# Performance work log

Hardware: AMD Instinct MI355X
Metric: run time of the kernel (lower is better)

## Reference

```python
import jax, jax.numpy as jnp
import numpy as np

FRAME = 1024
ENC = 256
HID = 128
EPS = 1e-7


def _lstm_cell(x, h, c, Wih, Whh, bih, bhh):
    # PyTorch LSTM gate order: i, f, g, o
    z = Wih @ x + bih + Whh @ h + bhh  # [4H]
    i, f, g, o = jnp.split(z, 4)
    i = jax.nn.sigmoid(i)
    f = jax.nn.sigmoid(f)
    g = jnp.tanh(g)
    o = jax.nn.sigmoid(o)
    c_new = f * c + i * g
    h_new = o * jnp.tanh(c_new)
    return h_new, c_new


def setup_inputs() -> dict:
    key = jax.random.key(0)
    ks = jax.random.split(key, 20)
    s = 0.05
    return {
        "y1": jax.random.normal(ks[0], (FRAME,), jnp.float32),
        "h1_in": jax.random.normal(ks[1], (HID,), jnp.float32),
        "c1_in": jax.random.normal(ks[2], (HID,), jnp.float32),
        "h2_in": jax.random.normal(ks[3], (HID,), jnp.float32),
        "c2_in": jax.random.normal(ks[4], (HID,), jnp.float32),
        "enc_W": jax.random.normal(ks[5], (ENC, FRAME), jnp.float32) * s,
        "gamma": jnp.ones((ENC,), jnp.float32),
        "beta": jnp.zeros((ENC,), jnp.float32),
        "Wih1": jax.random.normal(ks[6], (4 * HID, ENC), jnp.float32) * s,
        "Whh1": jax.random.normal(ks[7], (4 * HID, HID), jnp.float32) * s,
        "bih1": jax.random.normal(ks[8], (4 * HID,), jnp.float32) * s,
        "bhh1": jax.random.normal(ks[9], (4 * HID,), jnp.float32) * s,
        "Wih2": jax.random.normal(ks[10], (4 * HID, HID), jnp.float32) * s,
        "Whh2": jax.random.normal(ks[11], (4 * HID, HID), jnp.float32) * s,
        "bih2": jax.random.normal(ks[12], (4 * HID,), jnp.float32) * s,
        "bhh2": jax.random.normal(ks[13], (4 * HID,), jnp.float32) * s,
        "dense_W": jax.random.normal(ks[14], (ENC, HID), jnp.float32) * s,
        "dense_b": jax.random.normal(ks[15], (ENC,), jnp.float32) * s,
        "dec_W": jax.random.normal(ks[16], (FRAME, ENC), jnp.float32) * s,
    }


def reference(y1, h1_in, c1_in, h2_in, c2_in, enc_W, gamma, beta,
              Wih1, Whh1, bih1, bhh1, Wih2, Whh2, bih2, bhh2,
              dense_W, dense_b, dec_W):
    # encoder 1x1 conv == matvec: [256,1024] @ [1024]
    enc = enc_W @ y1  # [256]
    # global-statistic instant layer norm (mean/var over ALL elements)
    mean = jnp.mean(enc)
    sub = enc - mean
    var = jnp.mean(jnp.square(sub))
    enc_norm = (sub / jnp.sqrt(var + EPS)) * gamma + beta
    # two stateful LSTM cells (seq_len=1; dropout is identity at inference)
    h1, c1 = _lstm_cell(enc_norm, h1_in, c1_in, Wih1, Whh1, bih1, bhh1)
    h2, c2 = _lstm_cell(h1, h2_in, c2_in, Wih2, Whh2, bih2, bhh2)
    # dense + sigmoid mask on UN-normalized encoded features
    mask = jax.nn.sigmoid(dense_W @ h2 + dense_b)  # [256]
    estimated = mask * enc
    # decoder 1x1 conv == matvec: [1024,256] @ [256]
    decoded = dec_W @ estimated  # [1024]
    return (decoded.reshape(1, FRAME, 1),
            h1.reshape(1, 1, HID), c1.reshape(1, 1, HID),
            h2.reshape(1, 1, HID), c2.reshape(1, 1, HID))
```

## Files before the change

### kernel.cpp

```cpp
#include <hip/hip_runtime.h>
#include <math.h>


#define FRAME 1024
#define ENC 256
#define HID 128
#define MSTRIDE 32

__device__ __forceinline__ float sigmoidf_(float x) { return 1.0f / (1.0f + __expf(-x)); }
__device__ __forceinline__ float tanhf_(float x) { return 2.0f * sigmoidf_(2.0f * x) - 1.0f; }

__device__ __forceinline__ float wred(float v) {
#pragma unroll
    for (int o = 32; o > 0; o >>= 1) v += __shfl_xor(v, o);
    return v;
}

__global__ __launch_bounds__(256) void k_enc(
    const float* __restrict__ enc_W, const float* __restrict__ y1,
    const float* __restrict__ Whh1, const float* __restrict__ bih1,
    const float* __restrict__ bhh1, const float* __restrict__ h1_in,
    const float* __restrict__ Whh2, const float* __restrict__ bih2,
    const float* __restrict__ bhh2, const float* __restrict__ h2_in,
    float* __restrict__ enc_g, float* __restrict__ ph1,
    float* __restrict__ ph2, float* __restrict__ macc) {
    const int t = threadIdx.x, lane = t & 63, w = t >> 6, bid = blockIdx.x;
    if (bid < 256) {
        const float4 a = reinterpret_cast<const float4*>(enc_W + bid * FRAME)[t];
        const float4 b = reinterpret_cast<const float4*>(y1)[t];
        float p = a.x * b.x + a.y * b.y + a.z * b.z + a.w * b.w;
        p = wred(p);
        __shared__ float red[4];
        if (lane == 0) red[w] = p;
        __syncthreads();
        if (t == 0) enc_g[bid] = red[0] + red[1] + red[2] + red[3];
    } else {
        const bool is1 = bid < 288;
        const int pb = is1 ? bid - 256 : bid - 288;
        const float* Whh = is1 ? Whh1 : Whh2;
        const float* bi  = is1 ? bih1 : bih2;
        const float* bh  = is1 ? bhh1 : bhh2;
        const float* hin = is1 ? h1_in : h2_in;
        float* dst       = is1 ? ph1 : ph2;
        const float2 hv = reinterpret_cast<const float2*>(hin)[lane];
#pragma unroll
        for (int j = 0; j < 4; ++j) {
            const int r = pb * 16 + w * 4 + j;
            const float2 a = reinterpret_cast<const float2*>(Whh + r * HID)[lane];
            float p = a.x * hv.x + a.y * hv.y;
            p = wred(p);
            if (lane == 0) dst[r] = p + bi[r] + bh[r];
        }
        if (!is1 && t < 8) macc[(pb * 8 + t) * MSTRIDE] = 0.0f;
    }
}

__global__ __launch_bounds__(256) void k_z1(
    const float* __restrict__ enc_g, const float* __restrict__ gamma,
    const float* __restrict__ beta, const float* __restrict__ Wih1,
    const float* __restrict__ ph1, const float* __restrict__ c1_in,
    float* __restrict__ h1_g, float* __restrict__ out) {
    const int t = threadIdx.x, lane = t & 63, w = t >> 6, b = blockIdx.x;
    __shared__ __align__(16) float encN[ENC];
    __shared__ float red[8];
    __shared__ float zsh[4];

    const int r = b + HID * w;
    const float4 wa = reinterpret_cast<const float4*>(Wih1 + r * ENC)[lane];
    const float ph = ph1[r];

    const float e = enc_g[t];
    const float s1 = wred(e);
    const float s2 = wred(e * e);
    if (lane == 0) { red[w] = s1; red[4 + w] = s2; }
    __syncthreads();
    const float mean = (red[0] + red[1] + red[2] + red[3]) * (1.f / ENC);
    const float var  = (red[4] + red[5] + red[6] + red[7]) * (1.f / ENC) - mean * mean;
    const float inv  = rsqrtf(var + 1e-7f);
    encN[t] = (e - mean) * inv * gamma[t] + beta[t];
    __syncthreads();

    const float4 xa = reinterpret_cast<const float4*>(encN)[lane];
    float p = wa.x * xa.x + wa.y * xa.y + wa.z * xa.z + wa.w * xa.w;
    p = wred(p);
    if (lane == 0) zsh[w] = p + ph;
    __syncthreads();
    if (t == 0) {
        const float i = sigmoidf_(zsh[0]);
        const float f = sigmoidf_(zsh[1]);
        const float g = tanhf_(zsh[2]);
        const float o = sigmoidf_(zsh[3]);
        const float c = f * c1_in[b] + i * g;
        const float h = o * tanhf_(c);
        h1_g[b] = h;
        out[FRAME + b] = h;
        out[FRAME + HID + b] = c;
    }
}

__global__ __launch_bounds__(256) void k_z2(
    const float* __restrict__ h1_g, const float* __restrict__ Wih2,
    const float* __restrict__ ph2, const float* __restrict__ c2_in,
    const float* __restrict__ dense_W, float* __restrict__ macc,
    float* __restrict__ out) {
    const int t = threadIdx.x, lane = t & 63, w = t >> 6, bid = blockIdx.x;
    const int ub = bid * 4;
    __shared__ __align__(16) float hA[HID];
    __shared__ float zsh[16];
    __shared__ float h2sh[4];

    const float4 dcol = *reinterpret_cast<const float4*>(dense_W + t * HID + ub);
    float2 wa[4]; float phv[4];
#pragma unroll
    for (int j = 0; j < 4; ++j) {
        const int r = (ub + j) + HID * w;
        wa[j] = reinterpret_cast<const float2*>(Wih2 + r * HID)[lane];
        phv[j] = ph2[r];
    }

    if (t < HID) hA[t] = h1_g[t];
    __syncthreads();
    const float2 xa = reinterpret_cast<const float2*>(hA)[lane];
#pragma unroll
    for (int j = 0; j < 4; ++j) {
        float p = wa[j].x * xa.x + wa[j].y * xa.y;
        p = wred(p);
        if (lane == 0) zsh[w * 4 + j] = p + phv[j];
    }
    __syncthreads();
    if (t < 4) {
        const int u = ub + t;
        const float i = sigmoidf_(zsh[0 * 4 + t]);
        const float f = sigmoidf_(zsh[1 * 4 + t]);
        const float g = tanhf_(zsh[2 * 4 + t]);
        const float o = sigmoidf_(zsh[3 * 4 + t]);
        const float c = f * c2_in[u] + i * g;
        const float h = o * tanhf_(c);
        h2sh[t] = h;
        out[FRAME + 2 * HID + u] = h;
        out[FRAME + 3 * HID + u] = c;
    }
    __syncthreads();
    const float contrib = dcol.x * h2sh[0] + dcol.y * h2sh[1]
                        + dcol.z * h2sh[2] + dcol.w * h2sh[3];
    atomicAdd(&macc[t * MSTRIDE], contrib);
}

__global__ __launch_bounds__(256) void k_dec(
    const float* __restrict__ dec_W, const float* __restrict__ macc,
    const float* __restrict__ dense_b, const float* __restrict__ enc_g,
    float* __restrict__ out) {
    const int t = threadIdx.x, lane = t & 63, w = t >> 6;
    __shared__ __align__(16) float es[ENC];
    const float m = macc[t * MSTRIDE];
    es[t] = sigmoidf_(m + dense_b[t]) * enc_g[t];
    __syncthreads();
    const int r = blockIdx.x * 4 + w;
    const float4 a = reinterpret_cast<const float4*>(dec_W + r * ENC)[lane];
    const float4 bb = reinterpret_cast<const float4*>(es)[lane];
    float p = a.x * bb.x + a.y * bb.y + a.z * bb.z + a.w * bb.w;
    p = wred(p);
    if (lane == 0) out[r] = p;
}

extern "C" void kernel_launch(void* const* d_in, const int* in_sizes, int n_in,
                              void* d_out, int out_size, void* d_ws, size_t ws_size,
                              hipStream_t stream) {
    const float* y1      = (const float*)d_in[0];
    const float* h1_in   = (const float*)d_in[1];
    const float* c1_in   = (const float*)d_in[2];
    const float* h2_in   = (const float*)d_in[3];
    const float* c2_in   = (const float*)d_in[4];
    const float* enc_W   = (const float*)d_in[5];
    const float* gamma   = (const float*)d_in[6];
    const float* beta    = (const float*)d_in[7];
    const float* Wih1    = (const float*)d_in[8];
    const float* Whh1    = (const float*)d_in[9];
    const float* bih1    = (const float*)d_in[10];
    const float* bhh1    = (const float*)d_in[11];
    const float* Wih2    = (const float*)d_in[12];
    const float* Whh2    = (const float*)d_in[13];
    const float* bih2    = (const float*)d_in[14];
    const float* bhh2    = (const float*)d_in[15];
    const float* dense_W = (const float*)d_in[16];
    const float* dense_b = (const float*)d_in[17];
    const float* dec_W   = (const float*)d_in[18];

    float* out   = (float*)d_out;
    float* ws    = (float*)d_ws;
    float* enc_g = ws;
    float* h1_g  = ws + 256;
    float* macc  = ws + 512;
    float* ph1   = ws + 8704;
    float* ph2   = ws + 9216;

    k_enc<<<320, 256, 0, stream>>>(enc_W, y1, Whh1, bih1, bhh1, h1_in,
                                   Whh2, bih2, bhh2, h2_in, enc_g, ph1, ph2, macc);
    k_z1 <<<128, 256, 0, stream>>>(enc_g, gamma, beta, Wih1, ph1, c1_in, h1_g, out);
    k_z2 <<<32, 256, 0, stream>>>(h1_g, Wih2, ph2, c2_in, dense_W, macc, out);
    k_dec<<<256, 256, 0, stream>>>(dec_W, macc, dense_b, enc_g, out);
}
```

Measured before the change: 18.15 us.

## Fuse LSTM2 and decoder kernels with atomic flag-based grid synchronization

```diff
diff --git a/kernel.cpp b/kernel.cpp
--- a/kernel.cpp
+++ b/kernel.cpp
@@ -6,6 +6,9 @@
 #define ENC 256
 #define HID 128
 #define MSTRIDE 32
+#define NZ2 8
+#define UPB 16
+#define SCOPE __HIP_MEMORY_SCOPE_AGENT
 
 __device__ __forceinline__ float sigmoidf_(float x) { return 1.0f / (1.0f + __expf(-x)); }
 __device__ __forceinline__ float tanhf_(float x) { return 2.0f * sigmoidf_(2.0f * x) - 1.0f; }
@@ -23,7 +26,8 @@
     const float* __restrict__ Whh2, const float* __restrict__ bih2,
     const float* __restrict__ bhh2, const float* __restrict__ h2_in,
     float* __restrict__ enc_g, float* __restrict__ ph1,
-    float* __restrict__ ph2, float* __restrict__ macc) {
+    float* __restrict__ ph2, float* __restrict__ macc,
+    unsigned* __restrict__ ctr, unsigned* __restrict__ flag) {
     const int t = threadIdx.x, lane = t & 63, w = t >> 6, bid = blockIdx.x;
     if (bid < 256) {
         const float4 a = reinterpret_cast<const float4*>(enc_W + bid * FRAME)[t];
@@ -51,7 +55,15 @@
             p = wred(p);
             if (lane == 0) dst[r] = p + bi[r] + bh[r];
         }
-        if (!is1 && t < 8) macc[(pb * 8 + t) * MSTRIDE] = 0.0f;
+        if (!is1) {
+            if (t < 8) {
+                const int s = (pb * 8 + t) * MSTRIDE;
+                macc[s] = 0.0f;
+                ((unsigned*)macc)[s + 1] = 0u;
+            }
+            if (pb == 0 && t == 8) *ctr = 0u;
+            if (pb == 0 && t == 9) *flag = 0u;
+        }
     }
 }
 
@@ -98,69 +110,100 @@
     }
 }
 
-__global__ __launch_bounds__(256) void k_z2(
+__global__ __launch_bounds__(256) void k_tail(
     const float* __restrict__ h1_g, const float* __restrict__ Wih2,
     const float* __restrict__ ph2, const float* __restrict__ c2_in,
-    const float* __restrict__ dense_W, float* __restrict__ macc,
+    const float* __restrict__ dense_W, const float* __restrict__ dense_b,
+    const float* __restrict__ enc_g, const float* __restrict__ dec_W,
+    float* __restrict__ macc, float* __restrict__ est_g,
+    unsigned* __restrict__ ctr, unsigned* __restrict__ flag,
     float* __restrict__ out) {
     const int t = threadIdx.x, lane = t & 63, w = t >> 6, bid = blockIdx.x;
-    const int ub = bid * 4;
-    __shared__ __align__(16) float hA[HID];
-    __shared__ float zsh[16];
-    __shared__ float h2sh[4];
-
-    const float4 dcol = *reinterpret_cast<const float4*>(dense_W + t * HID + ub);
-    float2 wa[4]; float phv[4];
-#pragma unroll
-    for (int j = 0; j < 4; ++j) {
-        const int r = (ub + j) + HID * w;
-        wa[j] = reinterpret_cast<const float2*>(Wih2 + r * HID)[lane];
-        phv[j] = ph2[r];
+
+    if (bid < NZ2) {
+        __shared__ __align__(16) float hA[HID];
+        __shared__ float zsh[4][UPB];
+        __shared__ float h2sh[UPB];
+        const int ub = bid * UPB;
+        const int sub = lane >> 2, q = lane & 3;
+
+        const int r = (ub + sub) + HID * w;
+        float4 wa[8];
+        const float4* W4 = reinterpret_cast<const float4*>(Wih2 + r * HID) + q * 8;
+#pragma unroll
+        for (int i = 0; i < 8; ++i) wa[i] = W4[i];
+        const float phv = ph2[r];
+        float4 dcol[4];
+        const float4* D4 = reinterpret_cast<const float4*>(dense_W + t * HID + ub);
+#pragma unroll
+        for (int i = 0; i < 4; ++i) dcol[i] = D4[i];
+        const float dbv = dense_b[t];
+        const float ebv = enc_g[t];
+
+        if (t < HID) hA[t] = h1_g[t];
+        __syncthreads();
+        const float4* x4 = reinterpret_cast<const float4*>(hA) + q * 8;
+        float4 acc = {0.f, 0.f, 0.f, 0.f};
+#pragma unroll
+        for (int i = 0; i < 8; ++i) {
+            const float4 xv = x4[i];
+            acc.x += wa[i].x * xv.x; acc.y += wa[i].y * xv.y;
+            acc.z += wa[i].z * xv.z; acc.w += wa[i].w * xv.w;
+        }
+        float p = acc.x + acc.y + acc.z + acc.w;
+        p += __shfl_xor(p, 1); p += __shfl_xor(p, 2);
+        if (q == 0) zsh[w][sub] = p + phv;
+        __syncthreads();
+        if (t < UPB) {
+            const int u = ub + t;
+            const float i_ = sigmoidf_(zsh[0][t]);
+            const float f_ = sigmoidf_(zsh[1][t]);
+            const float g_ = tanhf_(zsh[2][t]);
+            const float o_ = sigmoidf_(zsh[3][t]);
+            const float c = f_ * c2_in[u] + i_ * g_;
+            const float h = o_ * tanhf_(c);
+            h2sh[t] = h;
+            out[FRAME + 2 * HID + u] = h;
+            out[FRAME + 3 * HID + u] = c;
+        }
+        __syncthreads();
+        float contrib = 0.f;
+#pragma unroll
+        for (int i = 0; i < 4; ++i) {
+            contrib += dcol[i].x * h2sh[i * 4 + 0] + dcol[i].y * h2sh[i * 4 + 1]
+                     + dcol[i].z * h2sh[i * 4 + 2] + dcol[i].w * h2sh[i * 4 + 3];
+        }
+        const float oldv = atomicAdd(&macc[t * MSTRIDE], contrib);
+        unsigned* mct = (unsigned*)&macc[t * MSTRIDE + 1];
+        const unsigned oc = __hip_atomic_fetch_add(mct, 1u, __ATOMIC_ACQ_REL, SCOPE);
+        if (oc == NZ2 - 1u) {
+            const float mfin = __hip_atomic_load(&macc[t * MSTRIDE], __ATOMIC_RELAXED, SCOPE);
+            (void)oldv;
+            const float e_ = sigmoidf_(mfin + dbv) * ebv;
+            __hip_atomic_store(&est_g[t], e_, __ATOMIC_RELAXED, SCOPE);
+        }
+        __syncthreads();
+        if (t == 0) {
+            const unsigned ob = __hip_atomic_fetch_add(ctr, 1u, __ATOMIC_ACQ_REL, SCOPE);
+            if (ob == NZ2 - 1u)
+                __hip_atomic_store(flag, 1u, __ATOMIC_RELEASE, SCOPE);
+        }
+    } else {
+        __shared__ __align__(16) float es[ENC];
+        const int r = (bid - NZ2) * 4 + w;
+        const float4 a = reinterpret_cast<const float4*>(dec_W + r * ENC)[lane];
+        if (t == 0) {
+            while (__hip_atomic_load(flag, __ATOMIC_ACQUIRE, SCOPE) == 0u)
+                __builtin_amdgcn_s_sleep(2);
+        }
+        __syncthreads();
+        es[t] = __hip_atomic_load(&est_g[t], __ATOMIC_RELAXED, SCOPE);
+        __syncthreads();
+        const float4 bb = reinterpret_cast<const float4*>(es)[lane];
+        float p = a.x * bb.x + a.y * bb.y + a.z * bb.z + a.w * bb.w;
+        p = wred(p);
+        if (lane == 0) out[r] = p;
     }
-
-    if (t < HID) hA[t] = h1_g[t];
-    __syncthreads();
-    const float2 xa = reinterpret_cast<const float2*>(hA)[lane];
-#pragma unroll
-    for (int j = 0; j < 4; ++j) {
-        float p = wa[j].x * xa.x + wa[j].y * xa.y;
-        p = wred(p);
-        if (lane == 0) zsh[w * 4 + j] = p + phv[j];
-    }
-    __syncthreads();
-    if (t < 4) {
-        const int u = ub + t;
-        const float i = sigmoidf_(zsh[0 * 4 + t]);
-        const float f = sigmoidf_(zsh[1 * 4 + t]);
-        const float g = tanhf_(zsh[2 * 4 + t]);
-        const float o = sigmoidf_(zsh[3 * 4 + t]);
-        const float c = f * c2_in[u] + i * g;
-        const float h = o * tanhf_(c);
-        h2sh[t] = h;
-        out[FRAME + 2 * HID + u] = h;
-        out[FRAME + 3 * HID + u] = c;
-    }
-    __syncthreads();
-    const float contrib = dcol.x * h2sh[0] + dcol.y * h2sh[1]
-                        + dcol.z * h2sh[2] + dcol.w * h2sh[3];
-    atomicAdd(&macc[t * MSTRIDE], contrib);
-}
-
-__global__ __launch_bounds__(256) void k_dec(
-    const float* __restrict__ dec_W, const float* __restrict__ macc,
-    const float* __restrict__ dense_b, const float* __restrict__ enc_g,
-    float* __restrict__ out) {
-    const int t = threadIdx.x, lane = t & 63, w = t >> 6;
-    __shared__ __align__(16) float es[ENC];
-    const float m = macc[t * MSTRIDE];
-    es[t] = sigmoidf_(m + dense_b[t]) * enc_g[t];
-    __syncthreads();
-    const int r = blockIdx.x * 4 + w;
-    const float4 a = reinterpret_cast<const float4*>(dec_W + r * ENC)[lane];
-    const float4 bb = reinterpret_cast<const float4*>(es)[lane];
-    float p = a.x * bb.x + a.y * bb.y + a.z * bb.z + a.w * bb.w;
-    p = wred(p);
-    if (lane == 0) out[r] = p;
 }
 
 extern "C" void kernel_launch(void* const* d_in, const int* in_sizes, int n_in,
@@ -193,10 +236,14 @@
     float* macc  = ws + 512;
     float* ph1   = ws + 8704;
     float* ph2   = ws + 9216;
-
-    k_enc<<<320, 256, 0, stream>>>(enc_W, y1, Whh1, bih1, bhh1, h1_in,
-                                   Whh2, bih2, bhh2, h2_in, enc_g, ph1, ph2, macc);
-    k_z1 <<<128, 256, 0, stream>>>(enc_g, gamma, beta, Wih1, ph1, c1_in, h1_g, out);
-    k_z2 <<<32, 256, 0, stream>>>(h1_g, Wih2, ph2, c2_in, dense_W, macc, out);
-    k_dec<<<256, 256, 0, stream>>>(dec_W, macc, dense_b, enc_g, out);
-}
+    float* est_g = ws + 9728;
+    unsigned* ctr  = (unsigned*)(ws + 9984);
+    unsigned* flag = (unsigned*)(ws + 10016);
+
+    k_enc <<<320, 256, 0, stream>>>(enc_W, y1, Whh1, bih1, bhh1, h1_in,
+                                    Whh2, bih2, bhh2, h2_in, enc_g, ph1, ph2,
+                                    macc, ctr, flag);
+    k_z1  <<<128, 256, 0, stream>>>(enc_g, gamma, beta, Wih1, ph1, c1_in, h1_g, out);
+    k_tail<<<264, 256, 0, stream>>>(h1_g, Wih2, ph2, c2_in, dense_W, dense_b,
+                                    enc_g, dec_W, macc, est_g, ctr, flag, out);
+}
```

Measured after the change: 61.70 us. +240.0%, slower.
